# Kernel optimization log

Measured on AMD Instinct MI355X. Metric: run time of the kernel, lower is better.

Reference implementation:

```python
import jax, jax.numpy as jnp
import numpy as np

B, S, D = 1, 2048, 1024
NH, HD, RD = 16, 64, 32        # nhead, head_dim, rope_dim (one head group)
KVC, QC = 256, 384             # kv / q compression dims
NSEQ = 4                       # len(tickers)
SPS = S // NSEQ                # seq_per_stock
LAMBDA_INIT = 0.8 - 0.6 * float(np.exp(-0.3 * 0))  # depth = 0 -> 0.2
EPS = 1e-5


def rmsnorm(x, w, eps=EPS):
    return x * jax.lax.rsqrt(jnp.mean(x * x, axis=-1, keepdims=True) + eps) * w


def setup_inputs() -> dict:
    key = jax.random.key(0)
    ks = jax.random.split(key, 12)
    w = lambda k, shape: jax.random.normal(k, shape, dtype=jnp.float32) * 0.02
    # causal mask, 1 (True) = masked; broadcast over head dim like torch masked_fill
    mask = jnp.triu(jnp.ones((S, S), dtype=bool), k=1)[None, None]
    # RoPE angles: dim = RD//2 = 16 half-dim rope features -> 8 complex freqs
    inv_freq = 1.0 / (10000.0 ** (np.arange(0, 16, 2, dtype=np.float32) / 16.0))
    freqs = jnp.asarray(np.outer(np.arange(SPS - 1, dtype=np.float32), inv_freq))
    return {
        "x": jax.random.normal(ks[0], (B, S, D), dtype=jnp.float32),
        "mask": mask,
        "freqs": freqs,
        "W_kv_down": w(ks[1], (D, KVC + RD)),
        "W_q_down": w(ks[2], (D, QC)),
        "kv_norm_w": jnp.ones((KVC,), jnp.float32),
        "q_norm_w": jnp.ones((QC,), jnp.float32),
        "W_kv_up": w(ks[3], (KVC, NH * HD * 2)),
        "W_q_up": w(ks[4], (QC, NH * (HD + RD))),
        "lambda_k1": jax.random.normal(ks[5], (HD // 2,), jnp.float32) * 0.1,
        "lambda_k2": jax.random.normal(ks[6], (HD // 2,), jnp.float32) * 0.1,
        "lambda_q1": jax.random.normal(ks[7], (HD // 2,), jnp.float32) * 0.1,
        "lambda_q2": jax.random.normal(ks[8], (HD // 2,), jnp.float32) * 0.1,
        "norm_w": jnp.ones((HD,), jnp.float32),
        "W_o": w(ks[9], (NH * HD, D)),
    }


def _rope_grouped(xr, freqs):
    # xr: [B, SPS, NSEQ, 2*NH, RD//2]; first token of each sub-sequence is kept
    # un-rotated (the 'separator'); remaining SPS-1 tokens get rotary embedding.
    head, rest = xr[:, :1], xr[:, 1:]
    r = rest.reshape(B, SPS - 1, NSEQ, 2 * NH, RD // 4, 2)
    cos = jnp.cos(freqs)[None, :, None, None, :]
    sin = jnp.sin(freqs)[None, :, None, None, :]
    a, b = r[..., 0], r[..., 1]
    rot = jnp.stack([a * cos - b * sin, a * sin + b * cos], axis=-1).reshape(rest.shape)
    return jnp.concatenate([head, rot], axis=1)


def reference(x, mask, freqs, W_kv_down, W_q_down, kv_norm_w, q_norm_w,
              W_kv_up, W_q_up, lambda_k1, lambda_k2, lambda_q1, lambda_q2,
              norm_w, W_o):
    # MLA down-projections + RMSNorm
    c = x @ W_kv_down                          # [B,S,KVC+RD]
    c_kv = rmsnorm(c[..., :KVC], kv_norm_w)
    k_rope_base = c[..., KVC:]                 # [B,S,RD]
    c_q = rmsnorm(x @ W_q_down, q_norm_w)

    # up-projections, split into paired half-dim heads (DINT)
    kv = (c_kv @ W_kv_up).reshape(B, S, NH, 2 * HD)
    k = kv[..., :HD].reshape(B, S, 2 * NH, HD // 2)
    v = kv[..., HD:]                           # [B,S,NH,HD]
    qp = (c_q @ W_q_up).reshape(B, S, NH, HD + RD)
    q = qp[..., :HD].reshape(B, S, 2 * NH, HD // 2)
    q_rope = qp[..., HD:].reshape(B, S, 2 * NH, RD // 2)
    k_rope = jnp.broadcast_to(k_rope_base[:, :, None, :], (B, S, NH, RD))
    k_rope = k_rope.reshape(B, S, 2 * NH, RD // 2)

    # per-sub-sequence RoPE (token t = p*NSEQ + s), vectorized over NSEQ
    q_rope = _rope_grouped(q_rope.reshape(B, SPS, NSEQ, 2 * NH, RD // 2), freqs)
    k_rope = _rope_grouped(k_rope.reshape(B, SPS, NSEQ, 2 * NH, RD // 2), freqs)
    q_rope = q_rope.reshape(B, S, 2 * NH, RD // 2)
    k_rope = k_rope.reshape(B, S, 2 * NH, RD // 2)

    q_f = jnp.concatenate([q, q_rope], -1).transpose(0, 2, 1, 3)  # [B,2NH,S,48]
    k_f = jnp.concatenate([k, k_rope], -1).transpose(0, 2, 1, 3)
    v_f = v.transpose(0, 2, 1, 3)                                 # [B,NH,S,HD]

    scale = ((HD + RD) // 2) ** (-0.5)
    a = jnp.einsum('bhqd,bhkd->bhqk', q_f, k_f) * scale
    abs_a = jnp.where(mask, -1e9, jnp.abs(a))
    a = jnp.sign(a) * jax.nn.softmax(abs_a, axis=-1)

    lam = (jnp.exp(jnp.sum(lambda_k1 * lambda_q1))
           - jnp.exp(jnp.sum(lambda_k2 * lambda_q2)) + LAMBDA_INIT)

    a = a.reshape(B, NH, 2, S, S)
    g = jnp.mean(a[:, :, 0], axis=-2, keepdims=True)   # [B,NH,1,S]
    a_final = a[:, :, 0] - lam * a[:, :, 1] + g * lam
    a_final = jnp.where(mask, 0.0, a_final)

    out = jnp.einsum('bhqk,bhkd->bhqd', a_final, v_f)  # [B,NH,S,HD]
    out = rmsnorm(out.transpose(0, 2, 1, 3), norm_w)   # [B,S,NH,HD]
    return out.reshape(B, S, NH * HD) @ W_o            # [B,S,D]
```

## Files before the change

kernel.cpp:

```cpp
#include <hip/hip_runtime.h>
#include <hip/hip_bf16.h>
#include <math.h>

constexpr int S    = 2048;
constexpr int D    = 1024;
constexpr int NH   = 16;
constexpr int H2   = 32;
constexpr int QKD  = 48;
constexpr int QKP  = 56;
constexpr int FCAP = 256;
constexpr float SCALE    = 0.14433756729740643f;
constexpr float LAM_INIT = 0.2f;
constexpr float EPS      = 1e-5f;
constexpr float THETA    = 1e-3f;

typedef __attribute__((ext_vector_type(8)))  short bf16x8;
typedef __attribute__((ext_vector_type(16))) float f32x16;

__device__ __forceinline__ int tile_order(int x) {
  return (x & 1) ? (31 - (x >> 1)) : (x >> 1);
}
__device__ __forceinline__ short f2bf(float x) {
  union { float f; unsigned u; } v; v.f = x;
  unsigned r = v.u + 0x7FFFu + ((v.u >> 16) & 1u);
  return (short)(r >> 16);
}
__device__ __forceinline__ float bf2f(short b) {
  union { unsigned u; float f; } v; v.u = ((unsigned)(unsigned short)b) << 16;
  return v.f;
}
__device__ __forceinline__ int d_rowpat(int r, int lane) {
  return (r & 3) + 8 * (r >> 2) + 4 * ((lane >> 5) & 1);
}
__device__ __forceinline__ f32x16 fzero16() {
  f32x16 z;
#pragma unroll
  for (int i = 0; i < 16; ++i) z[i] = 0.f;
  return z;
}
__device__ __forceinline__ bf16x8 frag56(const short* t, int lane, int sub, int ks) {
  return *(const bf16x8*)(t + ((lane & 31) + 32 * sub) * QKP + ((lane >> 5) << 3) + 16 * ks);
}
__device__ __forceinline__ bf16x8 frag72(const short* t, int lane, int sub, int ks) {
  return *(const bf16x8*)(t + ((lane & 31) + 32 * sub) * 72 + ((lane >> 5) << 3) + 16 * ks);
}
__device__ __forceinline__ f32x16 score_mfma(
    const short* ah, const short* al, const short* bh, const short* bl,
    int lane, int asub, int bsub) {
  f32x16 acc = fzero16();
#pragma unroll
  for (int t = 0; t < 3; ++t) {
    bf16x8 xh = frag56(ah, lane, asub, t);
    bf16x8 yh = frag56(bh, lane, bsub, t);
    bf16x8 xl = frag56(al, lane, asub, t);
    bf16x8 yl = frag56(bl, lane, bsub, t);
    acc = __builtin_amdgcn_mfma_f32_32x32x16_bf16(xh, yh, acc, 0, 0, 0);
    acc = __builtin_amdgcn_mfma_f32_32x32x16_bf16(xh, yl, acc, 0, 0, 0);
    acc = __builtin_amdgcn_mfma_f32_32x32x16_bf16(xl, yh, acc, 0, 0, 0);
  }
  return acc;
}
__device__ __forceinline__ void stage_tile(const unsigned* __restrict__ g,
                                           unsigned* __restrict__ lds, int tid) {
  for (int i = tid; i < 64 * 24; i += 256) {
    const int r = i / 24, c = i - r * 24;
    lds[r * 28 + c] = g[r * 24 + c];
  }
}
__device__ __forceinline__ void ldg_tile3(const unsigned* __restrict__ g,
                                          int tid, uint2 r[3]) {
  const uint2* g2 = (const uint2*)g;
#pragma unroll
  for (int j = 0; j < 3; ++j) r[j] = g2[tid + j * 256];
}
__device__ __forceinline__ void st_tile3(unsigned* __restrict__ lds,
                                         int tid, const uint2 r[3]) {
#pragma unroll
  for (int j = 0; j < 3; ++j) {
    const int e = 2 * (tid + j * 256);
    const int rr = e / 24, cc = e - rr * 24;
    *(uint2*)&lds[rr * 28 + cc] = r[j];
  }
}
__device__ __forceinline__ void ldg_t64(const unsigned* __restrict__ g,
                                        int ld_u2, int tid, uint2 r[4]) {
  const uint2* g2 = (const uint2*)g;
#pragma unroll
  for (int j = 0; j < 4; ++j) {
    const int e = tid + j * 256;
    const int row = e >> 4, c4 = e & 15;
    r[j] = g2[(size_t)row * ld_u2 + c4];
  }
}
__device__ __forceinline__ void st_t64(short* __restrict__ lds,
                                       int tid, const uint2 r[4]) {
#pragma unroll
  for (int j = 0; j < 4; ++j) {
    const int e = tid + j * 256;
    const int row = e >> 4, c4 = e & 15;
    *(uint2*)&lds[row * 72 + c4 * 4] = r[j];
  }
}
__device__ __forceinline__ void ldg_v4(const short* __restrict__ vb,
                                       int lane, int sub, int k0, bf16x8 r[4]) {
  const short* base = vb + ((size_t)((lane & 31) + 32 * sub)) * S + k0 +
                      ((lane >> 5) << 3);
#pragma unroll
  for (int t = 0; t < 4; ++t) r[t] = *(const bf16x8*)(base + 16 * t);
}
__device__ __forceinline__ float signedp(float sv, float mrow, float rrow) {
  const float e = __expf(fabsf(sv) - mrow) * rrow;
  return (sv > 0.f) ? e : ((sv < 0.f) ? -e : 0.f);
}
__device__ __forceinline__ float dot48(const float* __restrict__ a,
                                       const float* __restrict__ b) {
  float s = 0.f;
#pragma unroll
  for (int j = 0; j < 12; ++j) {
    float4 x = *(const float4*)&a[4 * j];
    float4 y = *(const float4*)&b[4 * j];
    s += x.x * y.x + x.y * y.y + x.z * y.z + x.w * y.w;
  }
  return s;
}

__global__ __launch_bounds__(256) void gemm_f32(
    const float* __restrict__ A, const float* __restrict__ B,
    float* __restrict__ C, int M, int K, int N) {
  __shared__ float As[16][64];
  __shared__ float Bs[16][128];
  const int tid = threadIdx.x;
  const int m0 = blockIdx.y * 64, n0 = blockIdx.x * 128;
  const int ty = tid >> 4, tx = tid & 15;
  float acc[4][8] = {};
  for (int k0 = 0; k0 < K; k0 += 16) {
    {
      const int am = tid >> 2;
      const int ak = (tid & 3) * 4;
      float4 a4 = *(const float4*)&A[(size_t)(m0 + am) * K + k0 + ak];
      As[ak + 0][am] = a4.x; As[ak + 1][am] = a4.y;
      As[ak + 2][am] = a4.z; As[ak + 3][am] = a4.w;
    }
#pragma unroll
    for (int it = 0; it < 2; ++it) {
      const int bk = (tid >> 5) + it * 8;
      const int bn = (tid & 31) * 4;
      const int gn = n0 + bn;
      float4 b4 = make_float4(0.f, 0.f, 0.f, 0.f);
      if (gn < N) b4 = *(const float4*)&B[(size_t)(k0 + bk) * N + gn];
      *(float4*)&Bs[bk][bn] = b4;
    }
    __syncthreads();
#pragma unroll
    for (int kk = 0; kk < 16; ++kk) {
      float a[4], b[8];
      *(float4*)&a[0] = *(const float4*)&As[kk][ty * 4];
      *(float4*)&b[0] = *(const float4*)&Bs[kk][tx * 8];
      *(float4*)&b[4] = *(const float4*)&Bs[kk][tx * 8 + 4];
#pragma unroll
      for (int r = 0; r < 4; ++r)
#pragma unroll
        for (int c = 0; c < 8; ++c) acc[r][c] += a[r] * b[c];
    }
    __syncthreads();
  }
#pragma unroll
  for (int r = 0; r < 4; ++r) {
    const int gm = m0 + ty * 4 + r;
#pragma unroll
    for (int c4 = 0; c4 < 2; ++c4) {
      const int gn = n0 + tx * 8 + c4 * 4;
      if (gn < N) {
        float4 v = make_float4(acc[r][c4 * 4], acc[r][c4 * 4 + 1],
                               acc[r][c4 * 4 + 2], acc[r][c4 * 4 + 3]);
        *(float4*)&C[(size_t)gm * N + gn] = v;
      }
    }
  }
}

__global__ __launch_bounds__(256) void rmsnorm_rows(
    const float* __restrict__ in, const float* __restrict__ w,
    float* __restrict__ out, int stride_in, int width) {
  const int row = blockIdx.x;
  const float* x = in + (size_t)row * stride_in;
  float ss = 0.f;
  for (int j = threadIdx.x; j < width; j += 256) { float v = x[j]; ss += v * v; }
  __shared__ float red[256];
  red[threadIdx.x] = ss;
  __syncthreads();
  for (int o = 128; o; o >>= 1) {
    if (threadIdx.x < o) red[threadIdx.x] += red[threadIdx.x + o];
    __syncthreads();
  }
  const float sc = rsqrtf(red[0] / (float)width + EPS);
  for (int j = threadIdx.x; j < width; j += 256)
    out[(size_t)row * width + j] = x[j] * sc * w[j];
}

__global__ __launch_bounds__(64) void assemble_qk(
    const float* __restrict__ qp, const float* __restrict__ kv,
    const float* __restrict__ c, const float* __restrict__ freqs,
    float* __restrict__ qfR, float* __restrict__ kfR,
    short* __restrict__ qhi, short* __restrict__ qlo,
    short* __restrict__ khi, short* __restrict__ klo) {
  const int h2 = blockIdx.x, s0 = blockIdx.y * 64;
  const int tid = threadIdx.x, s = s0 + tid;
  const int m = h2 >> 1, e = h2 & 1;
  const int sp = s >> 2;
  float cs[8], sn[8];
  if (sp > 0) {
#pragma unroll
    for (int t = 0; t < 8; ++t) {
      float a = freqs[(sp - 1) * 8 + t];
      cs[t] = cosf(a); sn[t] = sinf(a);
    }
  }
  float v[48], rr[16];
  {
    const float* qrow = qp + (size_t)s * (NH * 96) + m * 96;
#pragma unroll
    for (int j = 0; j < 32; ++j) v[j] = qrow[e * 32 + j];
#pragma unroll
    for (int j = 0; j < 16; ++j) rr[j] = qrow[64 + e * 16 + j];
    if (sp > 0) {
#pragma unroll
      for (int t = 0; t < 8; ++t) {
        float a = rr[2 * t], b = rr[2 * t + 1];
        rr[2 * t]     = a * cs[t] - b * sn[t];
        rr[2 * t + 1] = a * sn[t] + b * cs[t];
      }
    }
#pragma unroll
    for (int j = 0; j < 16; ++j) v[32 + j] = rr[j];
    float* dst = qfR + ((size_t)h2 * S + s) * 48;
#pragma unroll
    for (int j = 0; j < 12; ++j)
      *(float4*)&dst[4 * j] = make_float4(v[4 * j], v[4 * j + 1], v[4 * j + 2], v[4 * j + 3]);
    unsigned* dh = (unsigned*)(qhi + ((size_t)h2 * S + s) * 48);
    unsigned* dl = (unsigned*)(qlo + ((size_t)h2 * S + s) * 48);
#pragma unroll
    for (int j = 0; j < 24; ++j) {
      const short h0 = f2bf(v[2 * j]),     h1 = f2bf(v[2 * j + 1]);
      const short l0 = f2bf(v[2 * j] - bf2f(h0));
      const short l1 = f2bf(v[2 * j + 1] - bf2f(h1));
      dh[j] = (unsigned)(unsigned short)h0 | ((unsigned)(unsigned short)h1 << 16);
      dl[j] = (unsigned)(unsigned short)l0 | ((unsigned)(unsigned short)l1 << 16);
    }
  }
  {
    const float* krow = kv + (size_t)s * (NH * 128) + m * 128;
#pragma unroll
    for (int j = 0; j < 32; ++j) v[j] = krow[e * 32 + j];
#pragma unroll
    for (int j = 0; j < 16; ++j) rr[j] = c[(size_t)s * 288 + 256 + e * 16 + j];
    if (sp > 0) {
#pragma unroll
      for (int t = 0; t < 8; ++t) {
        float a = rr[2 * t], b = rr[2 * t + 1];
        rr[2 * t]     = a * cs[t] - b * sn[t];
        rr[2 * t + 1] = a * sn[t] + b * cs[t];
      }
    }
#pragma unroll
    for (int j = 0; j < 16; ++j) v[32 + j] = rr[j];
    float* dst = kfR + ((size_t)h2 * S + s) * 48;
#pragma unroll
    for (int j = 0; j < 12; ++j)
      *(float4*)&dst[4 * j] = make_float4(v[4 * j], v[4 * j + 1], v[4 * j + 2], v[4 * j + 3]);
    unsigned* dh = (unsigned*)(khi + ((size_t)h2 * S + s) * 48);
    unsigned* dl = (unsigned*)(klo + ((size_t)h2 * S + s) * 48);
#pragma unroll
    for (int j = 0; j < 24; ++j) {
      const short h0 = f2bf(v[2 * j]),     h1 = f2bf(v[2 * j + 1]);
      const short l0 = f2bf(v[2 * j] - bf2f(h0));
      const short l1 = f2bf(v[2 * j + 1] - bf2f(h1));
      dh[j] = (unsigned)(unsigned short)h0 | ((unsigned)(unsigned short)h1 << 16);
      dl[j] = (unsigned)(unsigned short)l0 | ((unsigned)(unsigned short)l1 << 16);
    }
  }
}

__global__ __launch_bounds__(256) void assemble_v(
    const float* __restrict__ kv, short* __restrict__ vThi,
    short* __restrict__ vTlo) {
  const int h = blockIdx.x, s0 = blockIdx.y * 64;
  const int tid = threadIdx.x;
  __shared__ float t[64][65];
  for (int i = tid; i < 4096; i += 256) {
    const int sl = i >> 6, dd = i & 63;
    t[sl][dd] = kv[(size_t)(s0 + sl) * (NH * 128) + h * 128 + 64 + dd];
  }
  __syncthreads();
  for (int i = tid; i < 4096; i += 256) {
    const int dd = i >> 6, sl = i & 63;
    const float v = t[sl][dd];
    const short hi = f2bf(v);
    vThi[((size_t)(h * 64 + dd)) * S + s0 + sl] = hi;
    vTlo[((size_t)(h * 64 + dd)) * S + s0 + sl] = f2bf(v - bf2f(hi));
  }
}

__global__ __launch_bounds__(256) void cvt_wo(
    const float* __restrict__ Wo, short* __restrict__ WoThi,
    short* __restrict__ WoTlo) {
  const int k0 = blockIdx.x * 64, n0 = blockIdx.y * 64;
  __shared__ float t[64][65];
  const int tid = threadIdx.x;
  for (int i = tid; i < 4096; i += 256) {
    const int kk = i >> 6, nn = i & 63;
    t[kk][nn] = Wo[(size_t)(k0 + kk) * D + n0 + nn];
  }
  __syncthreads();
  for (int i = tid; i < 4096; i += 256) {
    const int nn = i >> 6, kk = i & 63;
    const float v = t[kk][nn];
    const short hi = f2bf(v);
    WoThi[(size_t)(n0 + nn) * D + k0 + kk] = hi;
    WoTlo[(size_t)(n0 + nn) * D + k0 + kk] = f2bf(v - bf2f(hi));
  }
}

__global__ __launch_bounds__(64) void compute_lam(
    const float* __restrict__ lk1, const float* __restrict__ lk2,
    const float* __restrict__ lq1, const float* __restrict__ lq2,
    float* __restrict__ lam) {
  const int t = threadIdx.x;
  float p1 = (t < 32) ? lk1[t] * lq1[t] : 0.f;
  float p2 = (t < 32) ? lk2[t] * lq2[t] : 0.f;
  for (int o = 16; o; o >>= 1) {
    p1 += __shfl_down(p1, o);
    p2 += __shfl_down(p2, o);
  }
  if (t == 0) *lam = expf(p1) - expf(p2) + LAM_INIT;
}

__global__ __launch_bounds__(256) void attn_md(
    const short* __restrict__ qhi, const short* __restrict__ qlo,
    const short* __restrict__ khi, const short* __restrict__ klo,
    float* __restrict__ mOut, float* __restrict__ rdOut) {
  const int tile = tile_order(blockIdx.x), h2 = blockIdx.y;
  const int q0 = tile * 64;
  __shared__ __align__(16) short qh_s[64 * QKP], ql_s[64 * QKP];
  __shared__ __align__(16) short kh_s[64 * QKP], kl_s[64 * QKP];
  __shared__ float mpart[2][64], dpart[2][64];
  const int tid = threadIdx.x, lane = tid & 63, w = tid >> 6;
  const int asub = w >> 1, bsub = w & 1;
  stage_tile((const unsigned*)(qhi + ((size_t)h2 * S + q0) * 48), (unsigned*)qh_s, tid);
  stage_tile((const unsigned*)(qlo + ((size_t)h2 * S + q0) * 48), (unsigned*)ql_s, tid);
  uint2 kh_r[3], kl_r[3];
  ldg_tile3((const unsigned*)(khi + (size_t)h2 * S * 48), tid, kh_r);
  ldg_tile3((const unsigned*)(klo + (size_t)h2 * S * 48), tid, kl_r);
  float m_acc = -1e30f, d_acc = 0.f;
  const int qg = q0 + 32 * bsub + (lane & 31);
  for (int kt = 0; kt <= tile; ++kt) {
    const int k0 = kt * 64;
    st_tile3((unsigned*)kh_s, tid, kh_r);
    st_tile3((unsigned*)kl_s, tid, kl_r);
    if (kt < tile) {
      ldg_tile3((const unsigned*)(khi + ((size_t)h2 * S + k0 + 64) * 48), tid, kh_r);
      ldg_tile3((const unsigned*)(klo + ((size_t)h2 * S + k0 + 64) * 48), tid, kl_r);
    }
    __syncthreads();
    f32x16 acc = score_mfma(kh_s, kl_s, qh_s, ql_s, lane, asub, bsub);
    float av[16];
    float tm = -1e30f;
    if (kt < tile) {
#pragma unroll
      for (int r = 0; r < 16; ++r) { av[r] = fabsf(acc[r] * SCALE); tm = fmaxf(tm, av[r]); }
    } else {
#pragma unroll
      for (int r = 0; r < 16; ++r) {
        const int kg = k0 + 32 * asub + d_rowpat(r, lane);
        av[r] = (kg <= qg) ? fabsf(acc[r] * SCALE) : -1e30f;
        tm = fmaxf(tm, av[r]);
      }
    }
    const float nm = fmaxf(m_acc, tm);
    if (nm > -1e29f) {
      float add = 0.f;
#pragma unroll
      for (int r = 0; r < 16; ++r) add += __expf(av[r] - nm);
      d_acc = d_acc * __expf(m_acc - nm) + add;
      m_acc = nm;
    }
    __syncthreads();
  }
  {
    const float m2 = __shfl_xor(m_acc, 32);
    const float d2 = __shfl_xor(d_acc, 32);
    const float nm = fmaxf(m_acc, m2);
    float dd = 0.f;
    if (nm > -1e29f) dd = d_acc * __expf(m_acc - nm) + d2 * __expf(m2 - nm);
    if ((lane & 32) == 0) {
      mpart[asub][32 * bsub + (lane & 31)] = nm;
      dpart[asub][32 * bsub + (lane & 31)] = dd;
    }
  }
  __syncthreads();
  if (tid < 64) {
    const float ma = mpart[0][tid], mb = mpart[1][tid];
    const float da = dpart[0][tid], db = dpart[1][tid];
    const float mm = fmaxf(ma, mb);
    const float dsum = da * __expf(ma - mm) + db * __expf(mb - mm);
    mOut[h2 * S + q0 + tid] = mm;
    rdOut[h2 * S + q0 + tid] = 1.0f / dsum;
  }
}

__global__ __launch_bounds__(256) void attn_outp(
    const short* __restrict__ qhi, const short* __restrict__ qlo,
    const short* __restrict__ khi, const short* __restrict__ klo,
    const float* __restrict__ qfR, const float* __restrict__ kfR,
    const short* __restrict__ vThi, const short* __restrict__ vTlo,
    const float* __restrict__ mIn, const float* __restrict__ rdIn,
    float* __restrict__ opA0, float* __restrict__ opB0,
    float* __restrict__ opA1, float* __restrict__ opB1,
    float* __restrict__ gp) {
  const int tile = tile_order(blockIdx.x), h2 = blockIdx.y;
  const int chunk = blockIdx.z;
  const int h = h2 >> 1;
  const int q0 = tile * 64;
  __shared__ __align__(16) short qh_s[64 * QKP], ql_s[64 * QKP];
  __shared__ __align__(16) short kh_s[64 * QKP], kl_s[64 * QKP];
  __shared__ __align__(16) short ph_s[64 * 72], pl_s[64 * 72];
  __shared__ float mrow[64], rrow[64];
  __shared__ float gcol[2][64];
  __shared__ int fixq[FCAP];
  __shared__ int fixcnt;
  const int tid = threadIdx.x, lane = tid & 63, w = tid >> 6;
  const int qsub = w >> 1, sub2 = w & 1;
  const short* vbh = vThi + ((size_t)h * 64) * S;
  const short* vbl = vTlo + ((size_t)h * 64) * S;
  const float* qf = qfR + (size_t)h2 * S * 48;
  const float* kf = kfR + (size_t)h2 * S * 48;
  stage_tile((const unsigned*)(qhi + ((size_t)h2 * S + q0) * 48), (unsigned*)qh_s, tid);
  stage_tile((const unsigned*)(qlo + ((size_t)h2 * S + q0) * 48), (unsigned*)ql_s, tid);
  if (tid < 64) {
    mrow[tid] = mIn[h2 * S + q0 + tid];
    rrow[tid] = rdIn[h2 * S + q0 + tid];
  }
  uint2 kh_r[3], kl_r[3];
  bf16x8 vh_r[4], vl_r[4];
  const int kstart = (chunk <= tile) ? chunk : tile;
  ldg_tile3((const unsigned*)(khi + ((size_t)h2 * S + kstart * 64) * 48), tid, kh_r);
  ldg_tile3((const unsigned*)(klo + ((size_t)h2 * S + kstart * 64) * 48), tid, kl_r);
  ldg_v4(vbh, lane, sub2, kstart * 64, vh_r);
  ldg_v4(vbl, lane, sub2, kstart * 64, vl_r);
  f32x16 oacc = fzero16();
  const int colk = 32 * sub2 + (lane & 31);
  for (int kt = chunk; kt <= tile; kt += 2) {
    const int k0 = kt * 64;
    st_tile3((unsigned*)kh_s, tid, kh_r);
    st_tile3((unsigned*)kl_s, tid, kl_r);
    if (tid == 0) fixcnt = 0;
    if (kt + 2 <= tile) {
      ldg_tile3((const unsigned*)(khi + ((size_t)h2 * S + k0 + 128) * 48), tid, kh_r);
      ldg_tile3((const unsigned*)(klo + ((size_t)h2 * S + k0 + 128) * 48), tid, kl_r);
    }
    __syncthreads();
    f32x16 a = score_mfma(qh_s, ql_s, kh_s, kl_s, lane, qsub, sub2);
    const bool dg = (kt == tile);
    const int kg = k0 + colk;
    float colsum = 0.f;
#pragma unroll
    for (int r = 0; r < 16; ++r) {
      const int row = d_rowpat(r, lane) + 32 * qsub;
      float p = 0.f;
      if (!dg || kg <= (q0 + row)) {
        const float s = a[r];
        p = signedp(s * SCALE, mrow[row], rrow[row]);
        if (fabsf(s) < THETA) {
          const int sg = (s > 0.f) ? 1 : ((s < 0.f) ? 2 : 0);
          const int slot = atomicAdd(&fixcnt, 1);
          if (slot < FCAP) fixq[slot] = (row << 8) | (colk << 2) | sg;
        }
      }
      colsum += p;
      const short ph = f2bf(p);
      ph_s[row * 72 + colk] = ph;
      pl_s[row * 72 + colk] = f2bf(p - bf2f(ph));
    }
    colsum += __shfl_xor(colsum, 32);
    if ((lane & 32) == 0) gcol[qsub][colk] = colsum;
    __syncthreads();
    if ((h2 & 1) == 0 && tid < 64)
      gp[((size_t)(tile * NH + h)) * S + k0 + tid] = gcol[0][tid] + gcol[1][tid];
    if (fixcnt > 0) {
      const int cnt = min(fixcnt, FCAP);
#pragma unroll 1
      for (int i = tid; i < cnt; i += 256) {
        const int e = fixq[i];
        const int row = (e >> 8) & 63, ck = (e >> 2) & 63, sgc = e & 3;
        const float sgo = (sgc == 1) ? 1.f : ((sgc == 2) ? -1.f : 0.f);
        const float sx = dot48(qf + (size_t)(q0 + row) * 48,
                               kf + (size_t)(k0 + ck) * 48);
        const float sgn = (sx > 0.f) ? 1.f : ((sx < 0.f) ? -1.f : 0.f);
        if (sgn != sgo) {
          const float delta = (sgn - sgo) * __expf(-mrow[row]) * rrow[row];
          const int off = row * 72 + ck;
          const float pv = bf2f(ph_s[off]) + bf2f(pl_s[off]) + delta;
          const short nh = f2bf(pv);
          ph_s[off] = nh;
          pl_s[off] = f2bf(pv - bf2f(nh));
        }
      }
      __syncthreads();
    }
#pragma unroll
    for (int t = 0; t < 4; ++t) {
      bf16x8 pa = frag72(ph_s, lane, qsub, t);
      bf16x8 pl = frag72(pl_s, lane, qsub, t);
      oacc = __builtin_amdgcn_mfma_f32_32x32x16_bf16(pa, vh_r[t], oacc, 0, 0, 0);
      oacc = __builtin_amdgcn_mfma_f32_32x32x16_bf16(pa, vl_r[t], oacc, 0, 0, 0);
      oacc = __builtin_amdgcn_mfma_f32_32x32x16_bf16(pl, vh_r[t], oacc, 0, 0, 0);
    }
    if (kt + 2 <= tile) {
      ldg_v4(vbh, lane, sub2, k0 + 128, vh_r);
      ldg_v4(vbl, lane, sub2, k0 + 128, vl_r);
    }
  }
  float* op = (h2 & 1) ? (chunk ? opB1 : opB0) : (chunk ? opA1 : opA0);
#pragma unroll
  for (int r = 0; r < 16; ++r) {
    const int row = d_rowpat(r, lane) + 32 * qsub;
    op[((size_t)h * S + q0 + row) * 64 + colk] = oacc[r];
  }
}

__global__ __launch_bounds__(256) void g_reduce(
    const float* __restrict__ gp, float* __restrict__ g) {
  const int k = blockIdx.x * 256 + threadIdx.x;
  const int h = blockIdx.y;
  const int kt = k >> 6;
  float s = 0.f;
  for (int qt = kt; qt < 32; ++qt) s += gp[((size_t)(qt * NH + h)) * S + k];
  g[h * S + k] = s * (1.0f / (float)S);
}

__global__ __launch_bounds__(64) void gvc_scan1(
    const float* __restrict__ g, const short* __restrict__ vThi,
    const short* __restrict__ vTlo, float* __restrict__ gvc,
    float* __restrict__ csum) {
  const int chunk = blockIdx.x, h = blockIdx.y, dd = threadIdx.x;
  const int k0 = chunk * 64;
  const short* vh = vThi + ((size_t)(h * 64 + dd)) * S + k0;
  const short* vl = vTlo + ((size_t)(h * 64 + dd)) * S + k0;
  const float* gr = g + h * S + k0;
  float run = 0.f;
#pragma unroll 8
  for (int k = 0; k < 64; ++k) {
    run += gr[k] * (bf2f(vh[k]) + bf2f(vl[k]));
    gvc[((size_t)(h * S + k0 + k)) * 64 + dd] = run;
  }
  csum[((size_t)h * 32 + chunk) * 64 + dd] = run;
}
__global__ __launch_bounds__(64) void gvc_scan2(
    float* __restrict__ gvc, const float* __restrict__ csum) {
  const int chunk = blockIdx.x + 1, h = blockIdx.y, dd = threadIdx.x;
  float off = 0.f;
  for (int j = 0; j < chunk; ++j) off += csum[((size_t)h * 32 + j) * 64 + dd];
  const int k0 = chunk * 64;
#pragma unroll 8
  for (int k = 0; k < 64; ++k)
    gvc[((size_t)(h * S + k0 + k)) * 64 + dd] += off;
}

__global__ __launch_bounds__(256) void combine_out(
    const float* __restrict__ opA0, const float* __restrict__ opA1,
    const float* __restrict__ opB0, const float* __restrict__ opB1,
    const float* __restrict__ gvc, const float* __restrict__ lamPtr,
    const float* __restrict__ normW,
    short* __restrict__ nhi, short* __restrict__ nlo) {
  const int h = blockIdx.y, q0 = blockIdx.x * 64;
  const int tid = threadIdx.x, d = tid & 63, wv = tid >> 6;
  const float lam = *lamPtr;
  const float wn = normW[d];
#pragma unroll 4
  for (int i = 0; i < 16; ++i) {
    const int q = q0 + wv + 4 * i;
    const size_t off = ((size_t)h * S + q) * 64 + d;
    float val = (opA0[off] + opA1[off]) - lam * (opB0[off] + opB1[off])
              + lam * gvc[off];
    float ss = val * val;
#pragma unroll
    for (int o = 1; o < 64; o <<= 1) ss += __shfl_xor(ss, o);
    const float sc = rsqrtf(ss * (1.0f / 64.0f) + EPS);
    const float ov = val * sc * wn;
    const short hi = f2bf(ov);
    nhi[(size_t)q * D + h * 64 + d] = hi;
    nlo[(size_t)q * D + h * 64 + d] = f2bf(ov - bf2f(hi));
  }
}

__global__ __launch_bounds__(256) void gemm_bf16s(
    const short* __restrict__ Ahi, const short* __restrict__ Alo,
    const short* __restrict__ BThi, const short* __restrict__ BTlo,
    float* __restrict__ C) {
  const int n0 = blockIdx.x * 64, m0 = blockIdx.y * 64;
  __shared__ __align__(16) short ah_s[64 * 72], al_s[64 * 72];
  __shared__ __align__(16) short bh_s[64 * 72], bl_s[64 * 72];
  const int tid = threadIdx.x, lane = tid & 63, w = tid >> 6;
  const int msub = w >> 1, nsub = w & 1;
  uint2 ah_r[4], al_r[4], bh_r[4], bl_r[4];
  ldg_t64((const unsigned*)(Ahi + (size_t)m0 * D), 256, tid, ah_r);
  ldg_t64((const unsigned*)(Alo + (size_t)m0 * D), 256, tid, al_r);
  ldg_t64((const unsigned*)(BThi + (size_t)n0 * D), 256, tid, bh_r);
  ldg_t64((const unsigned*)(BTlo + (size_t)n0 * D), 256, tid, bl_r);
  f32x16 acc = fzero16();
  for (int kc = 0; kc < 16; ++kc) {
    st_t64(ah_s, tid, ah_r); st_t64(al_s, tid, al_r);
    st_t64(bh_s, tid, bh_r); st_t64(bl_s, tid, bl_r);
    if (kc < 15) {
      const int k0 = (kc + 1) * 64;
      ldg_t64((const unsigned*)(Ahi + (size_t)m0 * D + k0), 256, tid, ah_r);
      ldg_t64((const unsigned*)(Alo + (size_t)m0 * D + k0), 256, tid, al_r);
      ldg_t64((const unsigned*)(BThi + (size_t)n0 * D + k0), 256, tid, bh_r);
      ldg_t64((const unsigned*)(BTlo + (size_t)n0 * D + k0), 256, tid, bl_r);
    }
    __syncthreads();
#pragma unroll
    for (int t = 0; t < 4; ++t) {
      bf16x8 xh = frag72(ah_s, lane, msub, t);
      bf16x8 xl = frag72(al_s, lane, msub, t);
      bf16x8 yh = frag72(bh_s, lane, nsub, t);
      bf16x8 yl = frag72(bl_s, lane, nsub, t);
      acc = __builtin_amdgcn_mfma_f32_32x32x16_bf16(xh, yh, acc, 0, 0, 0);
      acc = __builtin_amdgcn_mfma_f32_32x32x16_bf16(xh, yl, acc, 0, 0, 0);
      acc = __builtin_amdgcn_mfma_f32_32x32x16_bf16(xl, yh, acc, 0, 0, 0);
    }
    __syncthreads();
  }
  const int col = 32 * nsub + (lane & 31);
#pragma unroll
  for (int r = 0; r < 16; ++r) {
    const int row = d_rowpat(r, lane) + 32 * msub;
    C[(size_t)(m0 + row) * D + n0 + col] = acc[r];
  }
}

extern "C" void kernel_launch(void* const* d_in, const int* in_sizes, int n_in,
                              void* d_out, int out_size, void* d_ws, size_t ws_size,
                              hipStream_t stream) {
  const float* x     = (const float*)d_in[0];
  const float* freqs = (const float*)d_in[2];
  const float* Wkvd  = (const float*)d_in[3];
  const float* Wqd   = (const float*)d_in[4];
  const float* kvnw  = (const float*)d_in[5];
  const float* qnw   = (const float*)d_in[6];
  const float* Wkvup = (const float*)d_in[7];
  const float* Wqup  = (const float*)d_in[8];
  const float* lk1   = (const float*)d_in[9];
  const float* lk2   = (const float*)d_in[10];
  const float* lq1   = (const float*)d_in[11];
  const float* lq2   = (const float*)d_in[12];
  const float* normw = (const float*)d_in[13];
  const float* Wo    = (const float*)d_in[14];
  float* out = (float*)d_out;

  float* ws = (float*)d_ws;
  float* c      = ws;
  float* ckv    = c     + (size_t)S * 288;
  float* cqr    = ckv   + (size_t)S * 256;
  float* cq     = cqr   + (size_t)S * 384;
  float* kvbuf  = cq    + (size_t)S * 384;
  float* qp     = kvbuf + (size_t)S * 2048;
  float* qfR    = qp    + (size_t)S * 1536;
  float* kfR    = qfR   + (size_t)H2 * S * 48;
  short* qhi    = (short*)(kfR + (size_t)H2 * S * 48);
  short* qlo    = qhi + (size_t)H2 * S * 48;
  short* khi    = qlo + (size_t)H2 * S * 48;
  short* klo    = khi + (size_t)H2 * S * 48;
  short* vThi   = klo + (size_t)H2 * S * 48;
  short* vTlo   = vThi + (size_t)NH * 64 * S;
  float* mbuf   = (float*)(vTlo + (size_t)NH * 64 * S);
  float* rdbuf  = mbuf  + (size_t)H2 * S;
  float* gbuf   = rdbuf + (size_t)H2 * S;
  float* lam    = gbuf  + (size_t)NH * S;
  float* csum   = lam + 1;
  float* opB1   = csum + (size_t)NH * 32 * 64;
  short* nhi    = (short*)(opB1 + (size_t)NH * S * 64);
  short* nlo    = nhi + (size_t)S * D;
  short* WoThi  = nlo + (size_t)S * D;
  short* WoTlo  = WoThi + (size_t)D * D;
  float* gvc    = kvbuf;
  float* opB0   = kvbuf + (size_t)NH * S * 64;
  float* opA0   = ckv;
  float* opA1   = qp;
  float* gp     = qp + (size_t)NH * S * 64;

  cvt_wo<<<dim3(16, 16), 256, 0, stream>>>(Wo, WoThi, WoTlo);
  gemm_f32<<<dim3(3, S / 64), 256, 0, stream>>>(x, Wkvd, c, S, D, 288);
  gemm_f32<<<dim3(3, S / 64), 256, 0, stream>>>(x, Wqd, cqr, S, D, 384);
  rmsnorm_rows<<<S, 256, 0, stream>>>(c, kvnw, ckv, 288, 256);
  rmsnorm_rows<<<S, 256, 0, stream>>>(cqr, qnw, cq, 384, 384);
  gemm_f32<<<dim3(16, S / 64), 256, 0, stream>>>(ckv, Wkvup, kvbuf, S, 256, 2048);
  gemm_f32<<<dim3(12, S / 64), 256, 0, stream>>>(cq, Wqup, qp, S, 384, 1536);
  assemble_qk<<<dim3(H2, S / 64), 64, 0, stream>>>(qp, kvbuf, c, freqs,
                                                   qfR, kfR, qhi, qlo, khi, klo);
  assemble_v<<<dim3(NH, S / 64), 256, 0, stream>>>(kvbuf, vThi, vTlo);
  compute_lam<<<1, 64, 0, stream>>>(lk1, lk2, lq1, lq2, lam);
  attn_md<<<dim3(32, H2), 256, 0, stream>>>(qhi, qlo, khi, klo, mbuf, rdbuf);
  attn_outp<<<dim3(32, H2, 2), 256, 0, stream>>>(qhi, qlo, khi, klo, qfR, kfR,
                                                 vThi, vTlo, mbuf, rdbuf,
                                                 opA0, opB0, opA1, opB1, gp);
  g_reduce<<<dim3(S / 256, NH), 256, 0, stream>>>(gp, gbuf);
  gvc_scan1<<<dim3(32, NH), 64, 0, stream>>>(gbuf, vThi, vTlo, gvc, csum);
  gvc_scan2<<<dim3(31, NH), 64, 0, stream>>>(gvc, csum);
  combine_out<<<dim3(S / 64, NH), 256, 0, stream>>>(opA0, opA1, opB0, opB1,
                                                    gvc, lam, normw, nhi, nlo);
  gemm_bf16s<<<dim3(D / 64, S / 64), 256, 0, stream>>>(nhi, nlo, WoThi, WoTlo, out);
}
```

Baseline: 787.3 us.

## Use single-bf16 scores in max/denominator pass and defer sign fixes to kernel

```diff
diff --git a/kernel.cpp b/kernel.cpp
--- a/kernel.cpp
+++ b/kernel.cpp
@@ -8,7 +8,7 @@
 constexpr int H2   = 32;
 constexpr int QKD  = 48;
 constexpr int QKP  = 56;
-constexpr int FCAP = 256;
+constexpr int QBUFCAP = 262144;
 constexpr float SCALE    = 0.14433756729740643f;
 constexpr float LAM_INIT = 0.2f;
 constexpr float EPS      = 1e-5f;
@@ -58,6 +58,15 @@
     acc = __builtin_amdgcn_mfma_f32_32x32x16_bf16(xh, yl, acc, 0, 0, 0);
     acc = __builtin_amdgcn_mfma_f32_32x32x16_bf16(xl, yh, acc, 0, 0, 0);
   }
+  return acc;
+}
+__device__ __forceinline__ f32x16 score_mfma1(
+    const short* a, const short* b, int lane, int asub, int bsub) {
+  f32x16 acc = fzero16();
+#pragma unroll
+  for (int t = 0; t < 3; ++t)
+    acc = __builtin_amdgcn_mfma_f32_32x32x16_bf16(
+        frag56(a, lane, asub, t), frag56(b, lane, bsub, t), acc, 0, 0, 0);
   return acc;
 }
 __device__ __forceinline__ void stage_tile(const unsigned* __restrict__ g,
@@ -336,33 +345,27 @@
 }
 
 __global__ __launch_bounds__(256) void attn_md(
-    const short* __restrict__ qhi, const short* __restrict__ qlo,
-    const short* __restrict__ khi, const short* __restrict__ klo,
+    const short* __restrict__ qhi, const short* __restrict__ khi,
     float* __restrict__ mOut, float* __restrict__ rdOut) {
   const int tile = tile_order(blockIdx.x), h2 = blockIdx.y;
   const int q0 = tile * 64;
-  __shared__ __align__(16) short qh_s[64 * QKP], ql_s[64 * QKP];
-  __shared__ __align__(16) short kh_s[64 * QKP], kl_s[64 * QKP];
+  __shared__ __align__(16) short qh_s[64 * QKP];
+  __shared__ __align__(16) short kh_s[64 * QKP];
   __shared__ float mpart[2][64], dpart[2][64];
   const int tid = threadIdx.x, lane = tid & 63, w = tid >> 6;
   const int asub = w >> 1, bsub = w & 1;
   stage_tile((const unsigned*)(qhi + ((size_t)h2 * S + q0) * 48), (unsigned*)qh_s, tid);
-  stage_tile((const unsigned*)(qlo + ((size_t)h2 * S + q0) * 48), (unsigned*)ql_s, tid);
-  uint2 kh_r[3], kl_r[3];
+  uint2 kh_r[3];
   ldg_tile3((const unsigned*)(khi + (size_t)h2 * S * 48), tid, kh_r);
-  ldg_tile3((const unsigned*)(klo + (size_t)h2 * S * 48), tid, kl_r);
   float m_acc = -1e30f, d_acc = 0.f;
   const int qg = q0 + 32 * bsub + (lane & 31);
   for (int kt = 0; kt <= tile; ++kt) {
     const int k0 = kt * 64;
     st_tile3((unsigned*)kh_s, tid, kh_r);
-    st_tile3((unsigned*)kl_s, tid, kl_r);
-    if (kt < tile) {
+    if (kt < tile)
       ldg_tile3((const unsigned*)(khi + ((size_t)h2 * S + k0 + 64) * 48), tid, kh_r);
-      ldg_tile3((const unsigned*)(klo + ((size_t)h2 * S + k0 + 64) * 48), tid, kl_r);
-    }
-    __syncthreads();
-    f32x16 acc = score_mfma(kh_s, kl_s, qh_s, ql_s, lane, asub, bsub);
+    __syncthreads();
+    f32x16 acc = score_mfma1(kh_s, qh_s, lane, asub, bsub);
     float av[16];
     float tm = -1e30f;
     if (kt < tile) {
@@ -411,12 +414,12 @@
 __global__ __launch_bounds__(256) void attn_outp(
     const short* __restrict__ qhi, const short* __restrict__ qlo,
     const short* __restrict__ khi, const short* __restrict__ klo,
-    const float* __restrict__ qfR, const float* __restrict__ kfR,
     const short* __restrict__ vThi, const short* __restrict__ vTlo,
     const float* __restrict__ mIn, const float* __restrict__ rdIn,
     float* __restrict__ opA0, float* __restrict__ opB0,
     float* __restrict__ opA1, float* __restrict__ opB1,
-    float* __restrict__ gp) {
+    float* __restrict__ gp, int* __restrict__ qcnt,
+    unsigned* __restrict__ qbuf) {
   const int tile = tile_order(blockIdx.x), h2 = blockIdx.y;
   const int chunk = blockIdx.z;
   const int h = h2 >> 1;
@@ -426,14 +429,10 @@
   __shared__ __align__(16) short ph_s[64 * 72], pl_s[64 * 72];
   __shared__ float mrow[64], rrow[64];
   __shared__ float gcol[2][64];
-  __shared__ int fixq[FCAP];
-  __shared__ int fixcnt;
   const int tid = threadIdx.x, lane = tid & 63, w = tid >> 6;
   const int qsub = w >> 1, sub2 = w & 1;
   const short* vbh = vThi + ((size_t)h * 64) * S;
   const short* vbl = vTlo + ((size_t)h * 64) * S;
-  const float* qf = qfR + (size_t)h2 * S * 48;
-  const float* kf = kfR + (size_t)h2 * S * 48;
   stage_tile((const unsigned*)(qhi + ((size_t)h2 * S + q0) * 48), (unsigned*)qh_s, tid);
   stage_tile((const unsigned*)(qlo + ((size_t)h2 * S + q0) * 48), (unsigned*)ql_s, tid);
   if (tid < 64) {
@@ -453,7 +452,6 @@
     const int k0 = kt * 64;
     st_tile3((unsigned*)kh_s, tid, kh_r);
     st_tile3((unsigned*)kl_s, tid, kl_r);
-    if (tid == 0) fixcnt = 0;
     if (kt + 2 <= tile) {
       ldg_tile3((const unsigned*)(khi + ((size_t)h2 * S + k0 + 128) * 48), tid, kh_r);
       ldg_tile3((const unsigned*)(klo + ((size_t)h2 * S + k0 + 128) * 48), tid, kl_r);
@@ -472,8 +470,10 @@
         p = signedp(s * SCALE, mrow[row], rrow[row]);
         if (fabsf(s) < THETA) {
           const int sg = (s > 0.f) ? 1 : ((s < 0.f) ? 2 : 0);
-          const int slot = atomicAdd(&fixcnt, 1);
-          if (slot < FCAP) fixq[slot] = (row << 8) | (colk << 2) | sg;
+          const unsigned idx = (unsigned)atomicAdd(qcnt, 1);
+          if (idx < QBUFCAP)
+            qbuf[idx] = ((unsigned)h2 << 24) | ((unsigned)(q0 + row) << 13) |
+                        ((unsigned)kg << 2) | (unsigned)sg;
         }
       }
       colsum += p;
@@ -486,27 +486,6 @@
     __syncthreads();
     if ((h2 & 1) == 0 && tid < 64)
       gp[((size_t)(tile * NH + h)) * S + k0 + tid] = gcol[0][tid] + gcol[1][tid];
-    if (fixcnt > 0) {
-      const int cnt = min(fixcnt, FCAP);
-#pragma unroll 1
-      for (int i = tid; i < cnt; i += 256) {
-        const int e = fixq[i];
-        const int row = (e >> 8) & 63, ck = (e >> 2) & 63, sgc = e & 3;
-        const float sgo = (sgc == 1) ? 1.f : ((sgc == 2) ? -1.f : 0.f);
-        const float sx = dot48(qf + (size_t)(q0 + row) * 48,
-                               kf + (size_t)(k0 + ck) * 48);
-        const float sgn = (sx > 0.f) ? 1.f : ((sx < 0.f) ? -1.f : 0.f);
-        if (sgn != sgo) {
-          const float delta = (sgn - sgo) * __expf(-mrow[row]) * rrow[row];
-          const int off = row * 72 + ck;
-          const float pv = bf2f(ph_s[off]) + bf2f(pl_s[off]) + delta;
-          const short nh = f2bf(pv);
-          ph_s[off] = nh;
-          pl_s[off] = f2bf(pv - bf2f(nh));
-        }
-      }
-      __syncthreads();
-    }
 #pragma unroll
     for (int t = 0; t < 4; ++t) {
       bf16x8 pa = frag72(ph_s, lane, qsub, t);
@@ -525,6 +504,37 @@
   for (int r = 0; r < 16; ++r) {
     const int row = d_rowpat(r, lane) + 32 * qsub;
     op[((size_t)h * S + q0 + row) * 64 + colk] = oacc[r];
+  }
+}
+
+__global__ __launch_bounds__(256) void fix_apply(
+    const int* __restrict__ qcnt, const unsigned* __restrict__ qbuf,
+    const float* __restrict__ qfR, const float* __restrict__ kfR,
+    const float* __restrict__ mIn, const float* __restrict__ rdIn,
+    const short* __restrict__ vThi, const short* __restrict__ vTlo,
+    float* __restrict__ opA0, float* __restrict__ opB0) {
+  const int n = min(*qcnt, QBUFCAP);
+  const int lane = threadIdx.x & 63;
+  const int wid = (blockIdx.x * 256 + threadIdx.x) >> 6;
+  const int nw = (gridDim.x * 256) >> 6;
+  for (int i = wid; i < n; i += nw) {
+    const unsigned e = qbuf[i];
+    const int sgc = e & 3;
+    const int k = (e >> 2) & 2047;
+    const int q = (e >> 13) & 2047;
+    const int h2 = (e >> 24) & 31;
+    const float sgo = (sgc == 1) ? 1.f : ((sgc == 2) ? -1.f : 0.f);
+    const float sx = dot48(qfR + ((size_t)h2 * S + q) * 48,
+                           kfR + ((size_t)h2 * S + k) * 48);
+    const float sgn = (sx > 0.f) ? 1.f : ((sx < 0.f) ? -1.f : 0.f);
+    if (sgn != sgo) {
+      const int h = h2 >> 1;
+      const float delta = (sgn - sgo) * __expf(-mIn[h2 * S + q]) * rdIn[h2 * S + q];
+      float* op = (h2 & 1) ? opB0 : opA0;
+      const float v = bf2f(vThi[((size_t)(h * 64 + lane)) * S + k]) +
+                      bf2f(vTlo[((size_t)(h * 64 + lane)) * S + k]);
+      atomicAdd(&op[((size_t)h * S + q) * 64 + lane], delta * v);
+    }
   }
 }
 
@@ -683,12 +693,15 @@
   short* nlo    = nhi + (size_t)S * D;
   short* WoThi  = nlo + (size_t)S * D;
   short* WoTlo  = WoThi + (size_t)D * D;
+  int*   qcnt   = (int*)(WoTlo + (size_t)D * D);
+  unsigned* qbuf = (unsigned*)(qcnt + 4);
   float* gvc    = kvbuf;
   float* opB0   = kvbuf + (size_t)NH * S * 64;
   float* opA0   = ckv;
   float* opA1   = qp;
   float* gp     = qp + (size_t)NH * S * 64;
 
+  hipMemsetAsync(qcnt, 0, sizeof(int), stream);
   cvt_wo<<<dim3(16, 16), 256, 0, stream>>>(Wo, WoThi, WoTlo);
   gemm_f32<<<dim3(3, S / 64), 256, 0, stream>>>(x, Wkvd, c, S, D, 288);
   gemm_f32<<<dim3(3, S / 64), 256, 0, stream>>>(x, Wqd, cqr, S, D, 384);
@@ -700,10 +713,13 @@
                                                    qfR, kfR, qhi, qlo, khi, klo);
   assemble_v<<<dim3(NH, S / 64), 256, 0, stream>>>(kvbuf, vThi, vTlo);
   compute_lam<<<1, 64, 0, stream>>>(lk1, lk2, lq1, lq2, lam);
-  attn_md<<<dim3(32, H2), 256, 0, stream>>>(qhi, qlo, khi, klo, mbuf, rdbuf);
-  attn_outp<<<dim3(32, H2, 2), 256, 0, stream>>>(qhi, qlo, khi, klo, qfR, kfR,
+  attn_md<<<dim3(32, H2), 256, 0, stream>>>(qhi, khi, mbuf, rdbuf);
+  attn_outp<<<dim3(32, H2, 2), 256, 0, stream>>>(qhi, qlo, khi, klo,
                                                  vThi, vTlo, mbuf, rdbuf,
-                                                 opA0, opB0, opA1, opB1, gp);
+                                                 opA0, opB0, opA1, opB1, gp,
+                                                 qcnt, qbuf);
+  fix_apply<<<256, 256, 0, stream>>>(qcnt, qbuf, qfR, kfR, mbuf, rdbuf,
+                                     vThi, vTlo, opA0, opB0);
   g_reduce<<<dim3(S / 256, NH), 256, 0, stream>>>(gp, gbuf);
   gvc_scan1<<<dim3(32, NH), 64, 0, stream>>>(gbuf, vThi, vTlo, gvc, csum);
   gvc_scan2<<<dim3(31, NH), 64, 0, stream>>>(gvc, csum);
```

Result: slower. 1.071 ms (+36.0%).
